# Kernel tuning notes

Measured on AMD Instinct MI355X. Metric: run time of the kernel, lower is better.

Reference implementation:

```python
import jax, jax.numpy as jnp
import numpy as np

NUM_HEADS = 16
KEY_SIZE = 64
D_MODEL = 1024


def setup_inputs() -> dict:
    key = jax.random.key(0)
    ks = jax.random.split(key, 9)
    B, S = 2, 2048
    HK = NUM_HEADS * KEY_SIZE
    s = 1.0 / np.sqrt(D_MODEL)
    return {
        "x": jax.random.normal(ks[0], (B, S, D_MODEL), dtype=jnp.float32),
        "Wq": jax.random.normal(ks[1], (D_MODEL, HK), dtype=jnp.float32) * s,
        "bq": jax.random.normal(ks[2], (HK,), dtype=jnp.float32) * 0.02,
        "Wk": jax.random.normal(ks[3], (D_MODEL, HK), dtype=jnp.float32) * s,
        "bk": jax.random.normal(ks[4], (HK,), dtype=jnp.float32) * 0.02,
        "Wv": jax.random.normal(ks[5], (D_MODEL, HK), dtype=jnp.float32) * s,
        "bv": jax.random.normal(ks[6], (HK,), dtype=jnp.float32) * 0.02,
        "Wo": jax.random.normal(ks[7], (HK, D_MODEL), dtype=jnp.float32) * s,
        "bo": jax.random.normal(ks[8], (D_MODEL,), dtype=jnp.float32) * 0.02,
    }


def reference(x, Wq, bq, Wk, bk, Wv, bv, Wo, bo):
    B, S, _ = x.shape
    H, K = NUM_HEADS, KEY_SIZE
    # QKV projections -> (B, H, S, K)
    def proj(W, b):
        return (x @ W + b).reshape(B, S, H, K).transpose(0, 2, 1, 3)
    q = proj(Wq, bq)
    k = proj(Wk, bk)
    v = proj(Wv, bv)
    scale = jnp.sqrt(jnp.float32(K))
    scores = jnp.einsum('bhsk,bhtk->bhst', q, k) / scale  # (B,H,S,S)
    attn = jax.nn.softmax(scores, axis=-1)
    out = jnp.einsum('bhst,bhtk->bhsk', attn, v)  # (B,H,S,K)
    out = out.transpose(0, 2, 1, 3).reshape(B, S, H * K)
    return out @ Wo + bo
```

## Files before the change

kernel.cpp:

```cpp
#include <hip/hip_runtime.h>


#define NH 16
#define KS 64
#define DM 1024
#define BB 2
#define SS 2048
#define NT (BB*SS)
#define HKD 1024
#define L2E 1.44269504088896340736f

typedef __attribute__((ext_vector_type(4))) float floatx4;
typedef __attribute__((ext_vector_type(8))) short short8;

__device__ __forceinline__ unsigned short f2b(float f) {
  unsigned u = __builtin_bit_cast(unsigned, f);
  u = (u + 0x7fffu + ((u >> 16) & 1u)) >> 16;
  return (unsigned short)u;
}

__device__ __forceinline__ floatx4 mfma16(short8 a, short8 b, floatx4 c) {
  return __builtin_amdgcn_mfma_f32_16x16x32_bf16(a, b, c, 0, 0, 0);
}

__device__ __forceinline__ void async16(const void* g, void* l) {
  __builtin_amdgcn_global_load_lds(
      (const __attribute__((address_space(1))) unsigned int*)g,
      (__attribute__((address_space(3))) unsigned int*)l, 16, 0, 0);
}

__global__ __launch_bounds__(256) void prep_kernel(
    const float* __restrict__ x,
    const float* __restrict__ Wq, const float* __restrict__ Wk,
    const float* __restrict__ Wv, const float* __restrict__ Wo,
    unsigned short* __restrict__ xb,
    unsigned short* __restrict__ wqt, unsigned short* __restrict__ wkt,
    unsigned short* __restrict__ wvt, unsigned short* __restrict__ wot) {
  int bid = blockIdx.x;
  if (bid < NT * DM / 1024) {
    int i = (bid * 256 + threadIdx.x) * 4;
    float4 v = *(const float4*)(x + i);
    ushort4 o;
    o.x = f2b(v.x); o.y = f2b(v.y); o.z = f2b(v.z); o.w = f2b(v.w);
    *(ushort4*)(xb + i) = o;
    return;
  }
  int b2 = bid - NT * DM / 1024;
  int z = b2 >> 8;
  const float* W; unsigned short* Wt;
  if (z == 0)      { W = Wq; Wt = wqt; }
  else if (z == 1) { W = Wk; Wt = wkt; }
  else if (z == 2) { W = Wv; Wt = wvt; }
  else             { W = Wo; Wt = wot; }
  __shared__ __align__(16) unsigned short tile[64][80];
  int k0 = (b2 & 15) * 64, n0 = ((b2 >> 4) & 15) * 64;
  int t = threadIdx.x;
  int c0 = (t & 15) * 4, r = t >> 4;
  #pragma unroll
  for (int p = 0; p < 4; ++p) {
    int rr = r + p * 16;
    float4 v = *(const float4*)(W + (k0 + rr) * DM + n0 + c0);
    tile[c0 + 0][rr] = f2b(v.x);
    tile[c0 + 1][rr] = f2b(v.y);
    tile[c0 + 2][rr] = f2b(v.z);
    tile[c0 + 3][rr] = f2b(v.w);
  }
  __syncthreads();
  int cc0 = (t & 7) * 8, rn = t >> 3;
  #pragma unroll
  for (int p = 0; p < 2; ++p) {
    int nn = rn + p * 32;
    *(short8*)(Wt + (n0 + nn) * DM + k0 + cc0) = *(const short8*)(&tile[nn][cc0]);
  }
}

__global__ __launch_bounds__(256) void gemm_qkv_kernel(
    const unsigned short* __restrict__ xb,
    const unsigned short* __restrict__ wqt, const unsigned short* __restrict__ wkt,
    const unsigned short* __restrict__ wvt,
    const float* __restrict__ bq, const float* __restrict__ bk, const float* __restrict__ bv,
    unsigned short* __restrict__ qb, unsigned short* __restrict__ kbuf,
    unsigned short* __restrict__ vt) {
  __shared__ __align__(16) unsigned short smem[18432];
  const unsigned short* Bt; const float* bias; float scale; int zid = blockIdx.z;
  if (zid == 0)      { Bt = wqt; bias = bq; scale = 0.125f * L2E; }
  else if (zid == 1) { Bt = wkt; bias = bk; scale = 1.0f; }
  else               { Bt = wvt; bias = bv; scale = 1.0f; }
  int m0 = blockIdx.x * 128, n0 = blockIdx.y * 128;
  int t = threadIdx.x, w = t >> 6, lane = t & 63, cl = lane & 15, quad = lane >> 4;
  int wr = (w >> 1) * 64, wc = (w & 1) * 64;
  floatx4 acc[4][4];
  #pragma unroll
  for (int i = 0; i < 4; ++i)
    #pragma unroll
    for (int j = 0; j < 4; ++j)
      acc[i][j] = floatx4{0.f, 0.f, 0.f, 0.f};

  auto stage = [&](int kc, int buf) {
    #pragma unroll
    for (int i = 0; i < 2; ++i) {
      int c = i * 256 + t;
      int row = c >> 2, col = (c & 3) ^ (row & 3);
      async16(xb + (m0 + row) * DM + kc * 32 + col * 8, &smem[buf * 4096 + c * 8]);
      async16(Bt + (n0 + row) * DM + kc * 32 + col * 8, &smem[8192 + buf * 4096 + c * 8]);
    }
  };
  stage(0, 0);
  stage(1, 1);

  for (int kc = 0; kc < DM / 32; ++kc) {
    int cur = kc & 1;
    if (kc < DM / 32 - 1) asm volatile("s_waitcnt vmcnt(4)" ::: "memory");
    else                  asm volatile("s_waitcnt vmcnt(0)" ::: "memory");
    __syncthreads();
    const unsigned short* Ac = &smem[cur * 4096];
    const unsigned short* Bc = &smem[8192 + cur * 4096];
    short8 a[4], b[4];
    #pragma unroll
    for (int i = 0; i < 4; ++i)
      a[i] = *(const short8*)&Ac[(wr + i * 16 + cl) * 32 + ((quad ^ (cl & 3)) * 8)];
    #pragma unroll
    for (int j = 0; j < 4; ++j)
      b[j] = *(const short8*)&Bc[(wc + j * 16 + cl) * 32 + ((quad ^ (cl & 3)) * 8)];
    #pragma unroll
    for (int i = 0; i < 4; ++i)
      #pragma unroll
      for (int j = 0; j < 4; ++j)
        acc[i][j] = mfma16(a[i], b[j], acc[i][j]);
    __syncthreads();
    if (kc + 2 < DM / 32) stage(kc + 2, cur);
  }
  __syncthreads();

  int h = (n0 + wc) >> 6;
  if (zid < 2) {
    unsigned short* dst = (zid == 0) ? qb : kbuf;
    #pragma unroll
    for (int j = 0; j < 4; ++j) {
      float bj = bias[n0 + wc + j * 16 + cl];
      int kd = j * 16 + cl;
      #pragma unroll
      for (int i = 0; i < 4; ++i)
        #pragma unroll
        for (int r = 0; r < 4; ++r) {
          int token = m0 + wr + i * 16 + quad * 4 + r;
          int bz = token >> 11, s = token & (SS - 1);
          float val = (acc[i][j][r] + bj) * scale;
          dst[(((bz * NH + h) * SS + s) << 6) + kd] = f2b(val);
        }
    }
  } else {
    unsigned short* tr = &smem[w * 4608];
    #pragma unroll
    for (int j = 0; j < 4; ++j) {
      float bj = bias[n0 + wc + j * 16 + cl];
      #pragma unroll
      for (int i = 0; i < 4; ++i) {
        unsigned short b0 = f2b(acc[i][j][0] + bj), b1 = f2b(acc[i][j][1] + bj);
        unsigned short b2 = f2b(acc[i][j][2] + bj), b3 = f2b(acc[i][j][3] + bj);
        uint2 pk;
        pk.x = (unsigned)b0 | ((unsigned)b1 << 16);
        pk.y = (unsigned)b2 | ((unsigned)b3 << 16);
        *(uint2*)&tr[(j * 16 + cl) * 72 + i * 16 + quad * 4] = pk;
      }
    }
    asm volatile("s_waitcnt lgkmcnt(0)" ::: "memory");
    int tokbase = m0 + wr;
    int bz = tokbase >> 11, s0 = tokbase & (SS - 1);
    unsigned short* vdst = vt + (((bz * NH + h) * KS) * SS) + s0;
    #pragma unroll
    for (int p = 0; p < 8; ++p) {
      int row = p * 8 + (lane >> 3);
      int tk = (lane & 7) * 8;
      short8 vv = *(const short8*)&tr[row * 72 + tk];
      *(short8*)(vdst + row * SS + tk) = vv;
    }
  }
}

__global__ __launch_bounds__(256) void attn_kernel(
    const unsigned short* __restrict__ Q, const unsigned short* __restrict__ Kb,
    const unsigned short* __restrict__ Vt, unsigned short* __restrict__ AO) {
  __shared__ __align__(16) unsigned short Ks[2][4096], Vs[2][4096];
  __shared__ __align__(16) unsigned short Ps[4][1024];
  int t = threadIdx.x, w = t >> 6, lane = t & 63, cl = lane & 15, quad = lane >> 4;
  int clm = cl & 7;
  int h = blockIdx.y, bz = blockIdx.z, bh = bz * NH + h;
  int q0 = blockIdx.x * 64 + w * 16;
  const unsigned short* Qp = Q + (bh * SS + q0) * KS;
  const unsigned short* Kp = Kb + bh * SS * KS;
  const unsigned short* Vp = Vt + bh * KS * SS;
  unsigned short* p_w = Ps[w];

  short8 qa[2];
  #pragma unroll
  for (int c = 0; c < 2; ++c)
    qa[c] = *(const short8*)(Qp + cl * KS + c * 32 + quad * 8);

  short8 ones;
  #pragma unroll
  for (int j = 0; j < 8; ++j) ones[j] = (short)0x3f80;

  floatx4 lacc = {0.f, 0.f, 0.f, 0.f};
  floatx4 oa[4];
  #pragma unroll
  for (int j = 0; j < 4; ++j) oa[j] = floatx4{0.f, 0.f, 0.f, 0.f};

  auto stage = [&](int tile, int buf) {
    const unsigned short* kp = Kp + (tile * 64) * KS;
    #pragma unroll
    for (int i = 0; i < 2; ++i) {
      int c = i * 256 + t;
      int row = c >> 3, col8 = (c & 7) ^ (row & 7);
      async16(kp + row * KS + col8 * 8, &Ks[buf][c * 8]);
    }
    #pragma unroll
    for (int i = 0; i < 2; ++i) {
      int c = i * 256 + t;
      int d = c >> 3, col8 = (c & 7) ^ (d & 7);
      async16(Vp + d * SS + tile * 64 + col8 * 8, &Vs[buf][c * 8]);
    }
  };
  stage(0, 0);
  stage(1, 1);

  const int NTILES = SS / 64;
  for (int it = 0; it < NTILES; ++it) {
    int cur = it & 1;
    if (it < NTILES - 1) asm volatile("s_waitcnt vmcnt(4)" ::: "memory");
    else                 asm volatile("s_waitcnt vmcnt(0)" ::: "memory");
    __syncthreads();

    floatx4 s[4];
    #pragma unroll
    for (int kt = 0; kt < 4; ++kt) {
      short8 kb0 = *(const short8*)&Ks[cur][(kt * 16 + cl) * 64 + ((quad ^ clm) * 8)];
      short8 kb1 = *(const short8*)&Ks[cur][(kt * 16 + cl) * 64 + (((4 + quad) ^ clm) * 8)];
      floatx4 z = {0.f, 0.f, 0.f, 0.f};
      s[kt] = mfma16(kb1, qa[1], mfma16(kb0, qa[0], z));
    }
    #pragma unroll
    for (int kt = 0; kt < 4; ++kt) {
      unsigned u[4];
      #pragma unroll
      for (int r = 0; r < 4; ++r)
        u[r] = __builtin_bit_cast(unsigned, __builtin_amdgcn_exp2f(s[kt][r]));
      uint2 pk;
      pk.x = __builtin_amdgcn_perm(u[1], u[0], 0x07060302);
      pk.y = __builtin_amdgcn_perm(u[3], u[2], 0x07060302);
      int off = cl * 64 + (((kt * 2 + (quad >> 1)) ^ clm) * 8) + (quad & 1) * 4;
      *(uint2*)(p_w + off) = pk;
    }
    asm volatile("s_waitcnt lgkmcnt(0)" ::: "memory");
    short8 pa[2];
    #pragma unroll
    for (int c = 0; c < 2; ++c)
      pa[c] = *(const short8*)(p_w + cl * 64 + (((c * 4 + quad) ^ clm) * 8));
    lacc = mfma16(ones, pa[1], mfma16(ones, pa[0], lacc));
    #pragma unroll
    for (int j = 0; j < 4; ++j) {
      short8 vb0 = *(const short8*)&Vs[cur][(j * 16 + cl) * 64 + ((quad ^ clm) * 8)];
      short8 vb1 = *(const short8*)&Vs[cur][(j * 16 + cl) * 64 + (((4 + quad) ^ clm) * 8)];
      oa[j] = mfma16(vb1, pa[1], mfma16(vb0, pa[0], oa[j]));
    }
    __syncthreads();
    if (it + 2 < NTILES) stage(it + 2, cur);
  }

  float inv = 1.0f / lacc[0];
  unsigned short* aop = AO + (bz * SS + q0 + cl) * DM + h * KS + quad * 4;
  #pragma unroll
  for (int j = 0; j < 4; ++j) {
    unsigned short b0 = f2b(oa[j][0] * inv), b1 = f2b(oa[j][1] * inv);
    unsigned short b2 = f2b(oa[j][2] * inv), b3 = f2b(oa[j][3] * inv);
    uint2 pk;
    pk.x = (unsigned)b0 | ((unsigned)b1 << 16);
    pk.y = (unsigned)b2 | ((unsigned)b3 << 16);
    *(uint2*)(aop + j * 16) = pk;
  }
}

__global__ __launch_bounds__(128) void gemm_out_kernel(
    const unsigned short* __restrict__ ao, const unsigned short* __restrict__ wot,
    const float* __restrict__ bo, float* __restrict__ out) {
  __shared__ __align__(16) unsigned short As[2][4096], Bs[2][2048];
  int m0 = blockIdx.x * 128, n0 = blockIdx.y * 64;
  int t = threadIdx.x, w = t >> 6, lane = t & 63, cl = lane & 15, quad = lane >> 4;
  int wr = w * 64;
  floatx4 acc[4][4];
  #pragma unroll
  for (int i = 0; i < 4; ++i)
    #pragma unroll
    for (int j = 0; j < 4; ++j)
      acc[i][j] = floatx4{0.f, 0.f, 0.f, 0.f};

  auto stage = [&](int kc, int buf) {
    #pragma unroll
    for (int i = 0; i < 4; ++i) {
      int c = i * 128 + t;
      int row = c >> 2, col = (c & 3) ^ (row & 3);
      async16(ao + (m0 + row) * HKD + kc * 32 + col * 8, &As[buf][c * 8]);
    }
    #pragma unroll
    for (int i = 0; i < 2; ++i) {
      int c = i * 128 + t;
      int row = c >> 2, col = (c & 3) ^ (row & 3);
      async16(wot + (n0 + row) * HKD + kc * 32 + col * 8, &Bs[buf][c * 8]);
    }
  };
  stage(0, 0);
  stage(1, 1);

  for (int kc = 0; kc < HKD / 32; ++kc) {
    int cur = kc & 1;
    if (kc < HKD / 32 - 1) asm volatile("s_waitcnt vmcnt(6)" ::: "memory");
    else                   asm volatile("s_waitcnt vmcnt(0)" ::: "memory");
    __syncthreads();
    short8 a[4], b[4];
    #pragma unroll
    for (int i = 0; i < 4; ++i)
      a[i] = *(const short8*)&As[cur][(wr + i * 16 + cl) * 32 + ((quad ^ (cl & 3)) * 8)];
    #pragma unroll
    for (int j = 0; j < 4; ++j)
      b[j] = *(const short8*)&Bs[cur][(j * 16 + cl) * 32 + ((quad ^ (cl & 3)) * 8)];
    #pragma unroll
    for (int i = 0; i < 4; ++i)
      #pragma unroll
      for (int j = 0; j < 4; ++j)
        acc[i][j] = mfma16(a[i], b[j], acc[i][j]);
    __syncthreads();
    if (kc + 2 < HKD / 32) stage(kc + 2, cur);
  }
  #pragma unroll
  for (int j = 0; j < 4; ++j) {
    float bj = bo[n0 + j * 16 + cl];
    #pragma unroll
    for (int i = 0; i < 4; ++i)
      #pragma unroll
      for (int r = 0; r < 4; ++r) {
        int token = m0 + wr + i * 16 + quad * 4 + r;
        out[token * DM + n0 + j * 16 + cl] = acc[i][j][r] + bj;
      }
  }
}

extern "C" void kernel_launch(void* const* d_in, const int* in_sizes, int n_in,
                              void* d_out, int out_size, void* d_ws, size_t ws_size,
                              hipStream_t stream) {
  const float* x  = (const float*)d_in[0];
  const float* Wq = (const float*)d_in[1];
  const float* bq = (const float*)d_in[2];
  const float* Wk = (const float*)d_in[3];
  const float* bk = (const float*)d_in[4];
  const float* Wv = (const float*)d_in[5];
  const float* bv = (const float*)d_in[6];
  const float* Wo = (const float*)d_in[7];
  const float* bo = (const float*)d_in[8];
  float* out = (float*)d_out;
  char* ws = (char*)d_ws;
  unsigned short* xb  = (unsigned short*)(ws);
  unsigned short* wqt = (unsigned short*)(ws + (8ull  << 20));
  unsigned short* wkt = (unsigned short*)(ws + (10ull << 20));
  unsigned short* wvt = (unsigned short*)(ws + (12ull << 20));
  unsigned short* wot = (unsigned short*)(ws + (14ull << 20));
  unsigned short* qb  = (unsigned short*)(ws + (16ull << 20));
  unsigned short* kbf = (unsigned short*)(ws + (24ull << 20));
  unsigned short* vt  = (unsigned short*)(ws + (40ull << 20));
  unsigned short* ao  = (unsigned short*)(ws + (48ull << 20));

  hipLaunchKernelGGL(prep_kernel, dim3(NT * DM / 1024 + 1024), dim3(256), 0, stream,
                     x, Wq, Wk, Wv, Wo, xb, wqt, wkt, wvt, wot);
  hipLaunchKernelGGL(gemm_qkv_kernel, dim3(NT / 128, HKD / 128, 3), dim3(256), 0, stream,
                     xb, wqt, wkt, wvt, bq, bk, bv, qb, kbf, vt);
  hipLaunchKernelGGL(attn_kernel, dim3(SS / 64, NH, BB), dim3(256), 0, stream, qb, kbf, vt, ao);
  hipLaunchKernelGGL(gemm_out_kernel, dim3(NT / 128, DM / 64), dim3(128), 0, stream, ao, wot, bo, out);
}
```

Measured before the change: 215.1 us.

## Double block sizes in attention and output GEMM, use raw barriers

```diff
diff --git a/kernel.cpp b/kernel.cpp
--- a/kernel.cpp
+++ b/kernel.cpp
@@ -12,6 +12,8 @@
 
 typedef __attribute__((ext_vector_type(4))) float floatx4;
 typedef __attribute__((ext_vector_type(8))) short short8;
+
+#define BAR() asm volatile("s_barrier" ::: "memory")
 
 __device__ __forceinline__ unsigned short f2b(float f) {
   unsigned u = __builtin_bit_cast(unsigned, f);
@@ -112,7 +114,7 @@
     int cur = kc & 1;
     if (kc < DM / 32 - 1) asm volatile("s_waitcnt vmcnt(4)" ::: "memory");
     else                  asm volatile("s_waitcnt vmcnt(0)" ::: "memory");
-    __syncthreads();
+    BAR();
     const unsigned short* Ac = &smem[cur * 4096];
     const unsigned short* Bc = &smem[8192 + cur * 4096];
     short8 a[4], b[4];
@@ -127,7 +129,7 @@
       #pragma unroll
       for (int j = 0; j < 4; ++j)
         acc[i][j] = mfma16(a[i], b[j], acc[i][j]);
-    __syncthreads();
+    BAR();
     if (kc + 2 < DM / 32) stage(kc + 2, cur);
   }
   __syncthreads();
@@ -178,15 +180,15 @@
   }
 }
 
-__global__ __launch_bounds__(256) void attn_kernel(
+__global__ __launch_bounds__(512) void attn_kernel(
     const unsigned short* __restrict__ Q, const unsigned short* __restrict__ Kb,
     const unsigned short* __restrict__ Vt, unsigned short* __restrict__ AO) {
   __shared__ __align__(16) unsigned short Ks[2][4096], Vs[2][4096];
-  __shared__ __align__(16) unsigned short Ps[4][1024];
+  __shared__ __align__(16) unsigned short Ps[8][1024];
   int t = threadIdx.x, w = t >> 6, lane = t & 63, cl = lane & 15, quad = lane >> 4;
   int clm = cl & 7;
   int h = blockIdx.y, bz = blockIdx.z, bh = bz * NH + h;
-  int q0 = blockIdx.x * 64 + w * 16;
+  int q0 = blockIdx.x * 128 + w * 16;
   const unsigned short* Qp = Q + (bh * SS + q0) * KS;
   const unsigned short* Kp = Kb + bh * SS * KS;
   const unsigned short* Vp = Vt + bh * KS * SS;
@@ -207,19 +209,9 @@
   for (int j = 0; j < 4; ++j) oa[j] = floatx4{0.f, 0.f, 0.f, 0.f};
 
   auto stage = [&](int tile, int buf) {
-    const unsigned short* kp = Kp + (tile * 64) * KS;
-    #pragma unroll
-    for (int i = 0; i < 2; ++i) {
-      int c = i * 256 + t;
-      int row = c >> 3, col8 = (c & 7) ^ (row & 7);
-      async16(kp + row * KS + col8 * 8, &Ks[buf][c * 8]);
-    }
-    #pragma unroll
-    for (int i = 0; i < 2; ++i) {
-      int c = i * 256 + t;
-      int d = c >> 3, col8 = (c & 7) ^ (d & 7);
-      async16(Vp + d * SS + tile * 64 + col8 * 8, &Vs[buf][c * 8]);
-    }
+    int row = t >> 3, col8 = (t & 7) ^ (row & 7);
+    async16(Kp + (tile * 64 + row) * KS + col8 * 8, &Ks[buf][t * 8]);
+    async16(Vp + row * SS + tile * 64 + col8 * 8, &Vs[buf][t * 8]);
   };
   stage(0, 0);
   stage(1, 1);
@@ -227,9 +219,9 @@
   const int NTILES = SS / 64;
   for (int it = 0; it < NTILES; ++it) {
     int cur = it & 1;
-    if (it < NTILES - 1) asm volatile("s_waitcnt vmcnt(4)" ::: "memory");
+    if (it < NTILES - 1) asm volatile("s_waitcnt vmcnt(2)" ::: "memory");
     else                 asm volatile("s_waitcnt vmcnt(0)" ::: "memory");
-    __syncthreads();
+    BAR();
 
     floatx4 s[4];
     #pragma unroll
@@ -263,7 +255,7 @@
       short8 vb1 = *(const short8*)&Vs[cur][(j * 16 + cl) * 64 + (((4 + quad) ^ clm) * 8)];
       oa[j] = mfma16(vb1, pa[1], mfma16(vb0, pa[0], oa[j]));
     }
-    __syncthreads();
+    BAR();
     if (it + 2 < NTILES) stage(it + 2, cur);
   }
 
@@ -280,11 +272,11 @@
   }
 }
 
-__global__ __launch_bounds__(128) void gemm_out_kernel(
+__global__ __launch_bounds__(256) void gemm_out_kernel(
     const unsigned short* __restrict__ ao, const unsigned short* __restrict__ wot,
     const float* __restrict__ bo, float* __restrict__ out) {
-  __shared__ __align__(16) unsigned short As[2][4096], Bs[2][2048];
-  int m0 = blockIdx.x * 128, n0 = blockIdx.y * 64;
+  __shared__ __align__(16) unsigned short As[2][8192], Bs[2][2048];
+  int m0 = blockIdx.x * 256, n0 = blockIdx.y * 64;
   int t = threadIdx.x, w = t >> 6, lane = t & 63, cl = lane & 15, quad = lane >> 4;
   int wr = w * 64;
   floatx4 acc[4][4];
@@ -297,13 +289,12 @@
   auto stage = [&](int kc, int buf) {
     #pragma unroll
     for (int i = 0; i < 4; ++i) {
-      int c = i * 128 + t;
+      int c = i * 256 + t;
       int row = c >> 2, col = (c & 3) ^ (row & 3);
       async16(ao + (m0 + row) * HKD + kc * 32 + col * 8, &As[buf][c * 8]);
     }
-    #pragma unroll
-    for (int i = 0; i < 2; ++i) {
-      int c = i * 128 + t;
+    {
+      int c = t;
       int row = c >> 2, col = (c & 3) ^ (row & 3);
       async16(wot + (n0 + row) * HKD + kc * 32 + col * 8, &Bs[buf][c * 8]);
     }
@@ -313,9 +304,9 @@
 
   for (int kc = 0; kc < HKD / 32; ++kc) {
     int cur = kc & 1;
-    if (kc < HKD / 32 - 1) asm volatile("s_waitcnt vmcnt(6)" ::: "memory");
+    if (kc < HKD / 32 - 1) asm volatile("s_waitcnt vmcnt(5)" ::: "memory");
     else                   asm volatile("s_waitcnt vmcnt(0)" ::: "memory");
-    __syncthreads();
+    BAR();
     short8 a[4], b[4];
     #pragma unroll
     for (int i = 0; i < 4; ++i)
@@ -328,7 +319,7 @@
       #pragma unroll
       for (int j = 0; j < 4; ++j)
         acc[i][j] = mfma16(a[i], b[j], acc[i][j]);
-    __syncthreads();
+    BAR();
     if (kc + 2 < HKD / 32) stage(kc + 2, cur);
   }
   #pragma unroll
@@ -372,6 +363,6 @@
                      x, Wq, Wk, Wv, Wo, xb, wqt, wkt, wvt, wot);
   hipLaunchKernelGGL(gemm_qkv_kernel, dim3(NT / 128, HKD / 128, 3), dim3(256), 0, stream,
                      xb, wqt, wkt, wvt, bq, bk, bv, qb, kbf, vt);
-  hipLaunchKernelGGL(attn_kernel, dim3(SS / 64, NH, BB), dim3(256), 0, stream, qb, kbf, vt, ao);
-  hipLaunchKernelGGL(gemm_out_kernel, dim3(NT / 128, DM / 64), dim3(128), 0, stream, ao, wot, bo, out);
-}
+  hipLaunchKernelGGL(attn_kernel, dim3(SS / 128, NH, BB), dim3(512), 0, stream, qb, kbf, vt, ao);
+  hipLaunchKernelGGL(gemm_out_kernel, dim3(NT / 256, DM / 64), dim3(256), 0, stream, ao, wot, bo, out);
+}
```

Measured after the change: 201.0 us. -6.5%, faster.
